# Optimization experiments

Hardware: AMD Instinct MI355X
Metric: run time of the kernel (lower is better)

## Reference

```python
import jax, jax.numpy as jnp
import numpy as np

N_NODES = 100000
N_EDGES = 1600000
IN_DIM = 128
HIDDEN = 16
OUT_DIM = 40
QMAX = 255.0  # 2**8 - 1


def quant_dequant(x, noise):
    """Per-row uint8 stochastic quantize + dequantize (straight-through in bwd)."""
    rmin = jnp.min(x, axis=1)  # [N]
    rmax = jnp.max(x, axis=1)  # [N]
    rscale = QMAX / (rmax - rmin)  # [N]
    q = (x - rmin[:, None]) * rscale[:, None]
    q = jnp.clip(jnp.round(q + noise - 0.5), 0.0, QMAX)
    q = q.astype(jnp.uint8).astype(x.dtype)  # uint8 storage as in torch code
    dq = q / rscale[:, None] + rmin[:, None]
    # straight-through: original custom backward ignores quantization
    return x + jax.lax.stop_gradient(dq - x)


def spmm(row, col, vals, x, n_nodes):
    """z[i] = sum_{e: row[e]==i} vals[e] * x[col[e]]  (COO A @ x)."""
    gathered = vals[:, None] * x[col]  # [E, d]
    return jax.ops.segment_sum(gathered, row, num_segments=n_nodes)


def gcn_layer(x, W, noise, row, col, vals):
    dq = quant_dequant(x, noise)
    z = spmm(row, col, vals, dq, x.shape[0])
    return z @ W


def setup_inputs() -> dict:
    key = jax.random.key(0)
    ks = jax.random.split(key, 10)
    features = jax.random.normal(ks[0], (N_NODES, IN_DIM), dtype=jnp.float32)
    row = jax.random.randint(ks[1], (N_EDGES,), 0, N_NODES, dtype=jnp.int32)
    col = jax.random.randint(ks[2], (N_EDGES,), 0, N_NODES, dtype=jnp.int32)
    vals = jax.random.uniform(ks[3], (N_EDGES,), dtype=jnp.float32)
    W1 = jax.random.normal(ks[4], (IN_DIM, HIDDEN), dtype=jnp.float32) * (1.0 / np.sqrt(IN_DIM))
    W2 = jax.random.normal(ks[5], (HIDDEN, HIDDEN), dtype=jnp.float32) * (1.0 / np.sqrt(HIDDEN))
    W3 = jax.random.normal(ks[6], (HIDDEN, OUT_DIM), dtype=jnp.float32) * (1.0 / np.sqrt(HIDDEN))
    noise1 = jax.random.uniform(ks[7], (N_NODES, IN_DIM), dtype=jnp.float32)
    noise2 = jax.random.uniform(ks[8], (N_NODES, HIDDEN), dtype=jnp.float32)
    noise3 = jax.random.uniform(ks[9], (N_NODES, HIDDEN), dtype=jnp.float32)
    return {"features": features, "row": row, "col": col, "vals": vals,
            "W1": W1, "W2": W2, "W3": W3,
            "noise1": noise1, "noise2": noise2, "noise3": noise3}


def reference(features, row, col, vals, W1, W2, W3, noise1, noise2, noise3):
    h = jax.nn.relu(gcn_layer(features, W1, noise1, row, col, vals))
    h = jax.nn.relu(gcn_layer(h, W2, noise2, row, col, vals))
    out = gcn_layer(h, W3, noise3, row, col, vals)
    return out
```

## Files before the change

kernel.cpp:

```cpp
#include <hip/hip_runtime.h>
#include <hip/hip_fp16.h>

#define N_NODES 100000
#define N_EDGES 1600000
#define IN_DIM 128
#define HIDDEN 16
#define OUT_DIM 40
#define QMAXF 255.0f

#define NB 512
#define RPB 196
#define NB_USED 511
#define BUCKET_CAP 4096
#define TILE 4096
#define EPT 16
#define NBLK_BIN ((N_EDGES + TILE - 1) / TILE)
#define HALF_CAP 2560
#define GEMM1_BLOCKS 1537

#define DQ_STRIDE 34
#define DQ_LEN 136

typedef float vfloat4 __attribute__((ext_vector_type(4)));

__device__ __forceinline__ float qd_one(float x, float noise, float rmin,
                                        float rscale, float inv) {
    float q = rintf((x - rmin) * rscale + noise - 0.5f);
    q = fminf(fmaxf(q, 0.0f), QMAXF);
    return q * inv + rmin;
}


__global__ __launch_bounds__(256) void k_bin(
    const int* __restrict__ row, const int* __restrict__ col,
    const float* __restrict__ vals, int* __restrict__ cursor,
    long long* __restrict__ es) {
    __shared__ int hist[NB];
    __shared__ int psum[256];
    __shared__ int lofs[NB];
    __shared__ int lcur[NB];
    __shared__ int gbase[NB];
    __shared__ long long stage[TILE];
    __shared__ int dsti[TILE];

    const int tid = threadIdx.x;
    for (int i = tid; i < NB; i += 256) hist[i] = 0;
    __syncthreads();

    int bk[EPT];
    long long ev[EPT];
    const int e0 = blockIdx.x * TILE;
#pragma unroll
    for (int k = 0; k < EPT; ++k) {
        const int e = e0 + k * 256 + tid;
        if (e < N_EDGES) {
            const int r = __builtin_nontemporal_load(row + e);
            const int cc = __builtin_nontemporal_load(col + e);
            const float vv = __builtin_nontemporal_load(vals + e);
            const int b = r / RPB;
            bk[k] = b;
            const unsigned lo = (unsigned)(cc | ((r - b * RPB) << 17));
            ev[k] = (long long)(((unsigned long long)__float_as_uint(vv) << 32) |
                                lo);
            atomicAdd(&hist[b], 1);
        } else {
            bk[k] = -1;
        }
    }
    __syncthreads();

    const int h0 = hist[2 * tid], h1 = hist[2 * tid + 1];
    psum[tid] = h0 + h1;
    __syncthreads();
    for (int off = 1; off < 256; off <<= 1) {
        int x = (tid >= off) ? psum[tid - off] : 0;
        __syncthreads();
        psum[tid] += x;
        __syncthreads();
    }
    const int excl = (tid == 0) ? 0 : psum[tid - 1];
    lofs[2 * tid] = excl;
    lofs[2 * tid + 1] = excl + h0;
    lcur[2 * tid] = excl;
    lcur[2 * tid + 1] = excl + h0;
    if (h0)
        gbase[2 * tid] = 2 * tid * BUCKET_CAP + atomicAdd(&cursor[2 * tid], h0);
    if (h1)
        gbase[2 * tid + 1] =
            (2 * tid + 1) * BUCKET_CAP + atomicAdd(&cursor[2 * tid + 1], h1);
    __syncthreads();

#pragma unroll
    for (int k = 0; k < EPT; ++k) {
        if (bk[k] >= 0) {
            const int b = bk[k];
            const int lp = atomicAdd(&lcur[b], 1);
            stage[lp] = ev[k];
            dsti[lp] = gbase[b] + (lp - lofs[b]);
        }
    }
    __syncthreads();

    const int S = psum[255];
    for (int i = tid; i < S; i += 256)
        __builtin_nontemporal_store(stage[i], es + dsti[i]);
}


struct SortLds {
    int hist[256];
    int psum[256];
    int cur[256];
};
union K1Lds {
    SortLds s;
    float dqbuf[4][DQ_LEN];
};

__global__ __launch_bounds__(256, 4) void k_sort_gemm1(
    const int* __restrict__ cursor, long long* __restrict__ es,
    int* __restrict__ rowEnd, const float* __restrict__ feat,
    const float* __restrict__ noise, const float* __restrict__ W1,
    __half* __restrict__ y) {
    __shared__ K1Lds u;
    const int tid = threadIdx.x;

    if (blockIdx.x < NB_USED) {
        const int b = blockIdx.x;
        const int start = b * BUCKET_CAP;
        const int cnt = cursor[b];

        u.s.hist[tid] = 0;
        __syncthreads();

        long long ev[EPT];
#pragma unroll
        for (int k = 0; k < EPT; ++k) {
            const int i = k * 256 + tid;
            if (i < cnt) {
                ev[k] = es[start + i];
                atomicAdd(&u.s.hist[(int)(((unsigned)ev[k]) >> 17)], 1);
            }
        }
        __syncthreads();

        u.s.psum[tid] = u.s.hist[tid];
        __syncthreads();
        for (int off = 1; off < 256; off <<= 1) {
            int x = (tid >= off) ? u.s.psum[tid - off] : 0;
            __syncthreads();
            u.s.psum[tid] += x;
            __syncthreads();
        }
        if (tid < RPB) rowEnd[b * RPB + tid] = start + u.s.psum[tid];
        u.s.cur[tid] = u.s.psum[tid] - u.s.hist[tid];
        __syncthreads();

#pragma unroll
        for (int k = 0; k < EPT; ++k) {
            const int i = k * 256 + tid;
            if (i < cnt) {
                const int r = (int)(((unsigned)ev[k]) >> 17);
                const int pos = atomicAdd(&u.s.cur[r], 1);
                es[start + pos] = ev[k];
            }
        }
    } else {
        const int vb = blockIdx.x - NB_USED;
        const int lane = tid & 63;
        const int wv = tid >> 6;
        const int col = lane & 15;
        const int kg = lane >> 4;
        const int kgw = lane >> 4;

        float w1r[32];
#pragma unroll
        for (int i = 0; i < 32; ++i) w1r[i] = W1[(kg * 32 + i) * HIDDEN + col];

        float* const myslice = u.dqbuf[wv];
        float2* const wptr =
            (float2*)&myslice[kgw * DQ_STRIDE + (lane & 15) * 2];
        const float* const dqk = &myslice[kg * DQ_STRIDE];

        const int ngroups = N_NODES / 4;
        for (int g = vb; g < ngroups; g += GEMM1_BLOCKS) {
            const int node = g * 4 + wv;
            const unsigned long long xr = __builtin_nontemporal_load(
                (const unsigned long long*)(feat + (size_t)node * IN_DIM) +
                lane);
            const unsigned long long nr = __builtin_nontemporal_load(
                (const unsigned long long*)(noise + (size_t)node * IN_DIM) +
                lane);
            const float xx = __uint_as_float((unsigned)xr);
            const float xy = __uint_as_float((unsigned)(xr >> 32));
            const float nx = __uint_as_float((unsigned)nr);
            const float ny = __uint_as_float((unsigned)(nr >> 32));
            float m = fminf(xx, xy), M = fmaxf(xx, xy);
#pragma unroll
            for (int off = 1; off < 64; off <<= 1) {
                m = fminf(m, __shfl_xor(m, off));
                M = fmaxf(M, __shfl_xor(M, off));
            }
            const float rscale = QMAXF / (M - m);
            const float inv = (M - m) / QMAXF;
            float2 dq;
            dq.x = qd_one(xx, nx, m, rscale, inv);
            dq.y = qd_one(xy, ny, m, rscale, inv);
            *wptr = dq;
            float acc = 0.0f;
#pragma unroll
            for (int i = 0; i < 32; ++i) acc += dqk[i] * w1r[i];
            acc += __shfl_xor(acc, 16);
            acc += __shfl_xor(acc, 32);
            if (lane < 16) y[(size_t)node * HIDDEN + lane] = __float2half(acc);
        }
    }
}


template <int LAYER>
__global__ __launch_bounds__(256, 4) void k_spmm_f(
    const int* __restrict__ rowEnd, const long long* __restrict__ es,
    const __half* __restrict__ y, const float* __restrict__ noise,
    const float* __restrict__ W, __half* __restrict__ yout,
    float* __restrict__ out) {
    __shared__ long long stage[HALF_CAP];
    __shared__ int rp[100];
    __shared__ int sh_se[2];
    __shared__ float wsh[LAYER == 1 ? (HIDDEN * HIDDEN)
                                    : (LAYER == 3 ? (HIDDEN * OUT_DIM) : 4)];

    const int b = blockIdx.x >> 1;
    const int hbk = blockIdx.x & 1;
    const int tid = threadIdx.x;
    const int r0 = hbk * 98;
    const int gb = b * RPB;
    const int bstart = b * BUCKET_CAP;

    if (tid == 0) {
        sh_se[0] = (r0 == 0) ? bstart : rowEnd[gb + r0 - 1];
        sh_se[1] = rowEnd[gb + r0 + 97];
    }
    if (tid < 99) rp[tid + 1] = rowEnd[gb + r0 + tid];
    if (LAYER == 1) {
        wsh[tid] = W[tid];
    }
    if (LAYER == 3) {
        for (int i = tid; i < HIDDEN * OUT_DIM; i += 256) wsh[i] = W[i];
    }
    __syncthreads();
    const int estart = sh_se[0];
    const int cnt = sh_se[1] - estart;
    if (tid == 0) rp[0] = estart;
    __syncthreads();

    for (int i = tid; i < cnt; i += 256)
        stage[i] = __builtin_nontemporal_load(es + estart + i);
    __syncthreads();

    if (tid >= 196) return;
    const int lr = tid >> 1;
    const int h = tid & 1;
    const int grow = gb + r0 + lr;
    int j = rp[lr] - estart;
    const int je = rp[lr + 1] - estart;

    float acc[8];
#pragma unroll
    for (int i = 0; i < 8; ++i) acc[i] = 0.0f;

    for (; j + 4 <= je; j += 4) {
        const long long e0 = stage[j], e1 = stage[j + 1];
        const long long e2 = stage[j + 2], e3 = stage[j + 3];
        const uint4 a0 = *(const uint4*)(y + (size_t)(((unsigned)e0) & 0x1FFFF) * HIDDEN + h * 8);
        const uint4 a1 = *(const uint4*)(y + (size_t)(((unsigned)e1) & 0x1FFFF) * HIDDEN + h * 8);
        const uint4 a2 = *(const uint4*)(y + (size_t)(((unsigned)e2) & 0x1FFFF) * HIDDEN + h * 8);
        const uint4 a3 = *(const uint4*)(y + (size_t)(((unsigned)e3) & 0x1FFFF) * HIDDEN + h * 8);
        const float v0 = __uint_as_float((unsigned)((unsigned long long)e0 >> 32));
        const float v1 = __uint_as_float((unsigned)((unsigned long long)e1 >> 32));
        const float v2 = __uint_as_float((unsigned)((unsigned long long)e2 >> 32));
        const float v3 = __uint_as_float((unsigned)((unsigned long long)e3 >> 32));
        const unsigned* p0 = (const unsigned*)&a0;
        const unsigned* p1 = (const unsigned*)&a1;
        const unsigned* p2 = (const unsigned*)&a2;
        const unsigned* p3 = (const unsigned*)&a3;
#pragma unroll
        for (int q = 0; q < 4; ++q) {
            float2 f;
            f = __half22float2(*(const __half2*)&p0[q]);
            acc[2 * q] += v0 * f.x; acc[2 * q + 1] += v0 * f.y;
            f = __half22float2(*(const __half2*)&p1[q]);
            acc[2 * q] += v1 * f.x; acc[2 * q + 1] += v1 * f.y;
            f = __half22float2(*(const __half2*)&p2[q]);
            acc[2 * q] += v2 * f.x; acc[2 * q + 1] += v2 * f.y;
            f = __half22float2(*(const __half2*)&p3[q]);
            acc[2 * q] += v3 * f.x; acc[2 * q + 1] += v3 * f.y;
        }
    }
    for (; j < je; ++j) {
        const long long e = stage[j];
        const float v = __uint_as_float((unsigned)((unsigned long long)e >> 32));
        const uint4 a = *(const uint4*)(y + (size_t)(((unsigned)e) & 0x1FFFF) * HIDDEN + h * 8);
        const unsigned* p = (const unsigned*)&a;
#pragma unroll
        for (int q = 0; q < 4; ++q) {
            const float2 f = __half22float2(*(const __half2*)&p[q]);
            acc[2 * q] += v * f.x;
            acc[2 * q + 1] += v * f.y;
        }
    }

    if (grow >= N_NODES) return;

    if (LAYER == 1 || LAYER == 2) {
#pragma unroll
        for (int i = 0; i < 8; ++i) acc[i] = fmaxf(acc[i], 0.0f);
        float m = acc[0], M = acc[0];
#pragma unroll
        for (int i = 1; i < 8; ++i) {
            m = fminf(m, acc[i]);
            M = fmaxf(M, acc[i]);
        }
        m = fminf(m, __shfl_xor(m, 1));
        M = fmaxf(M, __shfl_xor(M, 1));
        const float rscale = QMAXF / (M - m);
        const float inv = (M - m) / QMAXF;
        float nz[8];
        {
            const float4* nr =
                (const float4*)(noise + (size_t)grow * HIDDEN + h * 8);
            ((float4*)nz)[0] = nr[0];
            ((float4*)nz)[1] = nr[1];
        }
        float dq[8];
#pragma unroll
        for (int i = 0; i < 8; ++i)
            dq[i] = qd_one(acc[i], nz[i], m, rscale, inv);

        if (LAYER == 2) {
            __half hb8[8];
#pragma unroll
            for (int i = 0; i < 8; ++i) hb8[i] = __float2half(dq[i]);
            *(float4*)(yout + (size_t)grow * HIDDEN + h * 8) = *(float4*)hb8;
        } else {
            float dp[8];
#pragma unroll
            for (int i = 0; i < 8; ++i) dp[i] = __shfl_xor(dq[i], 1);
            const int kb = h * 8;
            const int pb = 8 - kb;
            const float* wmy = wsh + kb * HIDDEN + kb;
            const float* wpr = wsh + pb * HIDDEN + kb;
            float o[8];
#pragma unroll
            for (int jj = 0; jj < 8; ++jj) o[jj] = 0.0f;
#pragma unroll
            for (int i = 0; i < 8; ++i) {
#pragma unroll
                for (int jj = 0; jj < 8; ++jj) {
                    o[jj] += dq[i] * wmy[i * HIDDEN + jj];
                    o[jj] += dp[i] * wpr[i * HIDDEN + jj];
                }
            }
            __half hb8[8];
#pragma unroll
            for (int jj = 0; jj < 8; ++jj) hb8[jj] = __float2half(o[jj]);
            *(float4*)(yout + (size_t)grow * HIDDEN + kb) = *(float4*)hb8;
        }
    } else {
        float ap[8];
#pragma unroll
        for (int i = 0; i < 8; ++i) ap[i] = __shfl_xor(acc[i], 1);
        const int kb = h * 8;
        const int pb = 8 - kb;
        const int ob = h * 20;
        const float* wmy = wsh + kb * OUT_DIM + ob;
        const float* wpr = wsh + pb * OUT_DIM + ob;
        float o[20];
#pragma unroll
        for (int jj = 0; jj < 20; ++jj) o[jj] = 0.0f;
#pragma unroll
        for (int i = 0; i < 8; ++i) {
#pragma unroll
            for (int jj = 0; jj < 20; ++jj) {
                o[jj] += acc[i] * wmy[i * OUT_DIM + jj];
                o[jj] += ap[i] * wpr[i * OUT_DIM + jj];
            }
        }
        float* orow = out + (size_t)grow * OUT_DIM + ob;
#pragma unroll
        for (int j4 = 0; j4 < 5; ++j4)
            __builtin_nontemporal_store(((const vfloat4*)o)[j4],
                                        (vfloat4*)orow + j4);
    }
}

extern "C" void kernel_launch(void* const* d_in, const int* in_sizes, int n_in,
                              void* d_out, int out_size, void* d_ws,
                              size_t ws_size, hipStream_t stream) {
    const float* feat = (const float*)d_in[0];
    const int* row = (const int*)d_in[1];
    const int* col = (const int*)d_in[2];
    const float* vals = (const float*)d_in[3];
    const float* W1 = (const float*)d_in[4];
    const float* W2 = (const float*)d_in[5];
    const float* W3 = (const float*)d_in[6];
    const float* n1 = (const float*)d_in[7];
    const float* n2 = (const float*)d_in[8];
    const float* n3 = (const float*)d_in[9];
    float* out = (float*)d_out;

    __half* yh1 = (__half*)d_ws;
    __half* yh2 = yh1 + (size_t)N_NODES * HIDDEN;
    int* cursor = (int*)(yh2 + (size_t)N_NODES * HIDDEN);
    int* rowEnd = cursor + NB;
    long long* es = (long long*)(rowEnd + NB * RPB);

    hipMemsetAsync(cursor, 0, NB * sizeof(int), stream);
    k_bin<<<NBLK_BIN, 256, 0, stream>>>(row, col, vals, cursor, es);
    k_sort_gemm1<<<NB_USED + GEMM1_BLOCKS, 256, 0, stream>>>(
        cursor, es, rowEnd, feat, n1, W1, yh1);

    k_spmm_f<1><<<NB_USED * 2, 256, 0, stream>>>(rowEnd, es, yh1, n2, W2, yh2,
                                                 nullptr);
    k_spmm_f<2><<<NB_USED * 2, 256, 0, stream>>>(rowEnd, es, yh2, n3, nullptr,
                                                 yh1, nullptr);
    k_spmm_f<3><<<NB_USED * 2, 256, 0, stream>>>(rowEnd, es, yh1, nullptr, W3,
                                                 nullptr, out);
}
```

Before: 270.6 us.

## Fuse edge binning with layer-1 GEMM and split bucket sort into own kernel

```diff
diff --git a/kernel.cpp b/kernel.cpp
--- a/kernel.cpp
+++ b/kernel.cpp
@@ -12,8 +12,8 @@
 #define RPB 196
 #define NB_USED 511
 #define BUCKET_CAP 4096
-#define TILE 4096
-#define EPT 16
+#define TILE 1024
+#define EPT 4
 #define NBLK_BIN ((N_EDGES + TILE - 1) / TILE)
 #define HALF_CAP 2560
 #define GEMM1_BLOCKS 1537
@@ -31,155 +31,117 @@
 }
 
 
-__global__ __launch_bounds__(256) void k_bin(
+struct BinLds {
+    int hist[NB];
+    int psum[256];
+    int lofs[NB];
+    int lcur[NB];
+    int gbase[NB];
+    long long stage[TILE];
+    int dsti[TILE];
+};
+union K1Lds {
+    BinLds b;
+    float dqbuf[4][DQ_LEN];
+};
+
+__global__ __launch_bounds__(256, 4) void k_bin_gemm1(
     const int* __restrict__ row, const int* __restrict__ col,
     const float* __restrict__ vals, int* __restrict__ cursor,
-    long long* __restrict__ es) {
-    __shared__ int hist[NB];
-    __shared__ int psum[256];
-    __shared__ int lofs[NB];
-    __shared__ int lcur[NB];
-    __shared__ int gbase[NB];
-    __shared__ long long stage[TILE];
-    __shared__ int dsti[TILE];
-
-    const int tid = threadIdx.x;
-    for (int i = tid; i < NB; i += 256) hist[i] = 0;
-    __syncthreads();
-
-    int bk[EPT];
-    long long ev[EPT];
-    const int e0 = blockIdx.x * TILE;
-#pragma unroll
-    for (int k = 0; k < EPT; ++k) {
-        const int e = e0 + k * 256 + tid;
-        if (e < N_EDGES) {
-            const int r = __builtin_nontemporal_load(row + e);
-            const int cc = __builtin_nontemporal_load(col + e);
-            const float vv = __builtin_nontemporal_load(vals + e);
-            const int b = r / RPB;
-            bk[k] = b;
-            const unsigned lo = (unsigned)(cc | ((r - b * RPB) << 17));
-            ev[k] = (long long)(((unsigned long long)__float_as_uint(vv) << 32) |
-                                lo);
-            atomicAdd(&hist[b], 1);
-        } else {
-            bk[k] = -1;
-        }
-    }
-    __syncthreads();
-
-    const int h0 = hist[2 * tid], h1 = hist[2 * tid + 1];
-    psum[tid] = h0 + h1;
-    __syncthreads();
-    for (int off = 1; off < 256; off <<= 1) {
-        int x = (tid >= off) ? psum[tid - off] : 0;
-        __syncthreads();
-        psum[tid] += x;
-        __syncthreads();
-    }
-    const int excl = (tid == 0) ? 0 : psum[tid - 1];
-    lofs[2 * tid] = excl;
-    lofs[2 * tid + 1] = excl + h0;
-    lcur[2 * tid] = excl;
-    lcur[2 * tid + 1] = excl + h0;
-    if (h0)
-        gbase[2 * tid] = 2 * tid * BUCKET_CAP + atomicAdd(&cursor[2 * tid], h0);
-    if (h1)
-        gbase[2 * tid + 1] =
-            (2 * tid + 1) * BUCKET_CAP + atomicAdd(&cursor[2 * tid + 1], h1);
-    __syncthreads();
-
-#pragma unroll
-    for (int k = 0; k < EPT; ++k) {
-        if (bk[k] >= 0) {
-            const int b = bk[k];
-            const int lp = atomicAdd(&lcur[b], 1);
-            stage[lp] = ev[k];
-            dsti[lp] = gbase[b] + (lp - lofs[b]);
-        }
-    }
-    __syncthreads();
-
-    const int S = psum[255];
-    for (int i = tid; i < S; i += 256)
-        __builtin_nontemporal_store(stage[i], es + dsti[i]);
-}
-
-
-struct SortLds {
-    int hist[256];
-    int psum[256];
-    int cur[256];
-};
-union K1Lds {
-    SortLds s;
-    float dqbuf[4][DQ_LEN];
-};
-
-__global__ __launch_bounds__(256, 4) void k_sort_gemm1(
-    const int* __restrict__ cursor, long long* __restrict__ es,
-    int* __restrict__ rowEnd, const float* __restrict__ feat,
+    long long* __restrict__ es, const float* __restrict__ feat,
     const float* __restrict__ noise, const float* __restrict__ W1,
     __half* __restrict__ y) {
     __shared__ K1Lds u;
     const int tid = threadIdx.x;
 
-    if (blockIdx.x < NB_USED) {
-        const int b = blockIdx.x;
-        const int start = b * BUCKET_CAP;
-        const int cnt = cursor[b];
-
-        u.s.hist[tid] = 0;
-        __syncthreads();
-
+    const int bidx = blockIdx.x;
+    bool isBin;
+    int id;
+    if (bidx < 2 * GEMM1_BLOCKS) {
+        isBin = !(bidx & 1);
+        id = bidx >> 1;
+    } else {
+        isBin = true;
+        id = bidx - GEMM1_BLOCKS;
+    }
+
+    if (isBin) {
+        for (int i = tid; i < NB; i += 256) u.b.hist[i] = 0;
+        __syncthreads();
+
+        int bk[EPT];
         long long ev[EPT];
+        const int e0 = id * TILE;
 #pragma unroll
         for (int k = 0; k < EPT; ++k) {
-            const int i = k * 256 + tid;
-            if (i < cnt) {
-                ev[k] = es[start + i];
-                atomicAdd(&u.s.hist[(int)(((unsigned)ev[k]) >> 17)], 1);
+            const int e = e0 + k * 256 + tid;
+            if (e < N_EDGES) {
+                const int r = __builtin_nontemporal_load(row + e);
+                const int cc = __builtin_nontemporal_load(col + e);
+                const float vv = __builtin_nontemporal_load(vals + e);
+                const int b = r / RPB;
+                bk[k] = b;
+                const unsigned lo = (unsigned)(cc | ((r - b * RPB) << 17));
+                ev[k] = (long long)(
+                    ((unsigned long long)__float_as_uint(vv) << 32) | lo);
+                atomicAdd(&u.b.hist[b], 1);
+            } else {
+                bk[k] = -1;
             }
         }
         __syncthreads();
 
-        u.s.psum[tid] = u.s.hist[tid];
+        const int h0 = u.b.hist[2 * tid], h1 = u.b.hist[2 * tid + 1];
+        u.b.psum[tid] = h0 + h1;
         __syncthreads();
         for (int off = 1; off < 256; off <<= 1) {
-            int x = (tid >= off) ? u.s.psum[tid - off] : 0;
+            int x = (tid >= off) ? u.b.psum[tid - off] : 0;
             __syncthreads();
-            u.s.psum[tid] += x;
+            u.b.psum[tid] += x;
             __syncthreads();
         }
-        if (tid < RPB) rowEnd[b * RPB + tid] = start + u.s.psum[tid];
-        u.s.cur[tid] = u.s.psum[tid] - u.s.hist[tid];
+        const int excl = (tid == 0) ? 0 : u.b.psum[tid - 1];
+        u.b.lofs[2 * tid] = excl;
+        u.b.lofs[2 * tid + 1] = excl + h0;
+        u.b.lcur[2 * tid] = excl;
+        u.b.lcur[2 * tid + 1] = excl + h0;
+        if (h0)
+            u.b.gbase[2 * tid] =
+                2 * tid * BUCKET_CAP + atomicAdd(&cursor[2 * tid], h0);
+        if (h1)
+            u.b.gbase[2 * tid + 1] = (2 * tid + 1) * BUCKET_CAP +
+                                     atomicAdd(&cursor[2 * tid + 1], h1);
         __syncthreads();
 
 #pragma unroll
         for (int k = 0; k < EPT; ++k) {
-            const int i = k * 256 + tid;
-            if (i < cnt) {
-                const int r = (int)(((unsigned)ev[k]) >> 17);
-                const int pos = atomicAdd(&u.s.cur[r], 1);
-                es[start + pos] = ev[k];
+            if (bk[k] >= 0) {
+                const int b = bk[k];
+                const int lp = atomicAdd(&u.b.lcur[b], 1);
+                u.b.stage[lp] = ev[k];
+                u.b.dsti[lp] = u.b.gbase[b] + (lp - u.b.lofs[b]);
             }
         }
+        __syncthreads();
+
+        const int S = u.b.psum[255];
+        for (int i = tid; i < S; i += 256)
+            __builtin_nontemporal_store(u.b.stage[i], es + u.b.dsti[i]);
     } else {
-        const int vb = blockIdx.x - NB_USED;
+        const int vb = id;
         const int lane = tid & 63;
         const int wv = tid >> 6;
-        const int col = lane & 15;
+        const int col_ = lane & 15;
         const int kg = lane >> 4;
-        const int kgw = lane >> 4;
 
         float w1r[32];
 #pragma unroll
-        for (int i = 0; i < 32; ++i) w1r[i] = W1[(kg * 32 + i) * HIDDEN + col];
+        for (int i = 0; i < 32; ++i)
+            w1r[i] = W1[(kg * 32 + i) * HIDDEN + col_];
 
         float* const myslice = u.dqbuf[wv];
         float2* const wptr =
-            (float2*)&myslice[kgw * DQ_STRIDE + (lane & 15) * 2];
+            (float2*)&myslice[kg * DQ_STRIDE + (lane & 15) * 2];
         const float* const dqk = &myslice[kg * DQ_STRIDE];
 
         const int ngroups = N_NODES / 4;
@@ -213,6 +175,56 @@
             acc += __shfl_xor(acc, 16);
             acc += __shfl_xor(acc, 32);
             if (lane < 16) y[(size_t)node * HIDDEN + lane] = __float2half(acc);
+        }
+    }
+}
+
+
+__global__ __launch_bounds__(256, 4) void k_sort(
+    const int* __restrict__ cursor, long long* __restrict__ es,
+    int* __restrict__ rowEnd) {
+    __shared__ int hist[256];
+    __shared__ int psum[256];
+    __shared__ int cur[256];
+
+    const int b = blockIdx.x;
+    const int tid = threadIdx.x;
+    const int start = b * BUCKET_CAP;
+    const int cnt = cursor[b];
+
+    hist[tid] = 0;
+    __syncthreads();
+
+    long long ev[16];
+#pragma unroll
+    for (int k = 0; k < 16; ++k) {
+        const int i = k * 256 + tid;
+        if (i < cnt) {
+            ev[k] = es[start + i];
+            atomicAdd(&hist[(int)(((unsigned)ev[k]) >> 17)], 1);
+        }
+    }
+    __syncthreads();
+
+    psum[tid] = hist[tid];
+    __syncthreads();
+    for (int off = 1; off < 256; off <<= 1) {
+        int x = (tid >= off) ? psum[tid - off] : 0;
+        __syncthreads();
+        psum[tid] += x;
+        __syncthreads();
+    }
+    if (tid < RPB) rowEnd[b * RPB + tid] = start + psum[tid];
+    cur[tid] = psum[tid] - hist[tid];
+    __syncthreads();
+
+#pragma unroll
+    for (int k = 0; k < 16; ++k) {
+        const int i = k * 256 + tid;
+        if (i < cnt) {
+            const int r = (int)(((unsigned)ev[k]) >> 17);
+            const int pos = atomicAdd(&cur[r], 1);
+            es[start + pos] = ev[k];
         }
     }
 }
@@ -416,9 +428,9 @@
     long long* es = (long long*)(rowEnd + NB * RPB);
 
     hipMemsetAsync(cursor, 0, NB * sizeof(int), stream);
-    k_bin<<<NBLK_BIN, 256, 0, stream>>>(row, col, vals, cursor, es);
-    k_sort_gemm1<<<NB_USED + GEMM1_BLOCKS, 256, 0, stream>>>(
-        cursor, es, rowEnd, feat, n1, W1, yh1);
+    k_bin_gemm1<<<NBLK_BIN + GEMM1_BLOCKS, 256, 0, stream>>>(
+        row, col, vals, cursor, es, feat, n1, W1, yh1);
+    k_sort<<<NB_USED, 256, 0, stream>>>(cursor, es, rowEnd);
 
     k_spmm_f<1><<<NB_USED * 2, 256, 0, stream>>>(rowEnd, es, yh1, n2, W2, yh2,
                                                  nullptr);
```

Result: slower. 291.3 us (+7.7%).
